# Kernel tuning notes

Measured on AMD Instinct MI355X. Metric: run time of the kernel, lower is better.

The kernel has to match this reference:

```python
import jax, jax.numpy as jnp
import numpy as np

B, N = 16, 2048
EMB_DIM = 512
K = 20          # neighbor_num
S = 1           # support_num

def _norm(x, axis):
    # F.normalize: x / max(||x||, 1e-12)
    return x / jnp.maximum(jnp.linalg.norm(x, axis=axis, keepdims=True), 1e-12)

def knn(verts, k):
    # verts: (b, v, 3); squared-distance knn excluding self
    inner = jnp.einsum('bvd,bwd->bvw', verts, verts)
    quad = jnp.sum(verts * verts, axis=2)
    dist = quad[:, :, None] - 2.0 * inner + quad[:, None, :]
    _, idx = jax.lax.top_k(-dist, k + 1)
    return idx[:, :, 1:]

def gather_nb(x, idx):
    # x: (b, v, c), idx: (b, v, n) -> (b, v, n, c)
    return jax.vmap(lambda t, i: t[i])(x, idx)

def dir_norm(verts, idx):
    d = gather_nb(verts, idx) - verts[:, :, None, :]
    return _norm(d, -1)

def conv_surface(idx, verts, directions, kernel_num):
    theta = jax.nn.relu(jnp.einsum('bvnd,dk->bvnk', dir_norm(verts, idx), _norm(directions, 0)))
    b, v, n, _ = theta.shape
    theta = theta.reshape(b, v, n, S, kernel_num)
    return jnp.sum(jnp.max(theta, axis=2), axis=2)  # (b, v, kernel_num)

def conv_layer(idx, verts, fm, w, bias, directions, out_ch):
    theta = jax.nn.relu(jnp.einsum('bvnd,dk->bvnk', dir_norm(verts, idx), _norm(directions, 0)))
    feat = fm @ w + bias                            # (b, v, (S+1)*out_ch)
    center = feat[:, :, :out_ch]
    support = gather_nb(feat[:, :, out_ch:], idx)   # (b, v, n, S*out_ch)
    b, v, n, _ = support.shape
    act = (theta * support).reshape(b, v, n, S, out_ch)
    return center + jnp.sum(jnp.max(act, axis=2), axis=2)

def pool_layer(verts, fm, key, pooling_rate=4, neighbor_num=4):
    b, v, _ = verts.shape
    idx = knn(verts, neighbor_num)
    pooled = jnp.max(gather_nb(fm, idx), axis=2)
    samp = jax.random.permutation(key, v)[: v // pooling_rate]
    return verts[:, samp, :], pooled[:, samp, :]

def _forward(xyz, w1, b1, w2, b2, w3, b3, w4, b4, fcw, fcb, dir0,
             wc1, bc1, dir1, wc2, bc2, dir2, wc3, bc3, dir3, wc4, bc4, dir4,
             clw1, clb1, bn_gamma, bn_beta, clw2, clb2):
    relu = jax.nn.relu
    # PointNet trunk (Conv1d with kernel 1 == per-point matmul)
    x = relu(jnp.einsum('oc,bcn->bon', w1, xyz) + b1[None, :, None])
    x = relu(jnp.einsum('oc,bcn->bon', w2, x) + b2[None, :, None])
    gf = jnp.max(x, axis=2, keepdims=True)
    x = jnp.concatenate([x, jnp.broadcast_to(gf, x.shape)], axis=1)
    x = relu(jnp.einsum('oc,bcn->bon', w3, x) + b3[None, :, None])
    x = relu(jnp.einsum('oc,bcn->bon', w4, x) + b4[None, :, None])
    x = jnp.max(x, axis=2)                          # (B, 1024)
    # GCN3D trunk
    verts = jnp.transpose(xyz, (0, 2, 1))           # (B, N, 3)
    idx = knn(verts, K)
    fm0 = relu(conv_surface(idx, verts, dir0, 32))
    fm1 = relu(conv_layer(idx, verts, fm0, wc1, bc1, dir1, 64))
    verts, fm1 = pool_layer(verts, fm1, jax.random.key(1))
    idx = knn(verts, K)
    fm2 = relu(conv_layer(idx, verts, fm1, wc2, bc2, dir2, 128))
    fm3 = relu(conv_layer(idx, verts, fm2, wc3, bc3, dir3, 256))
    verts, fm3 = pool_layer(verts, fm3, jax.random.key(2))
    idx = knn(verts, K)
    fm4 = conv_layer(idx, verts, fm3, wc4, bc4, dir4, 1024)
    fg = jnp.max(fm4, axis=1)                       # (B, 1024)
    fc_data = jnp.concatenate([x, fg], axis=1)      # (B, 2048)
    embedding = fc_data @ fcw.T + fcb
    # classifier, eval mode: Dropout -> identity; BN uses running mean 0 / var 1
    h = fc_data @ clw1.T + clb1
    h = relu(h / jnp.sqrt(1.0 + 1e-5) * bn_gamma + bn_beta)
    pred = h @ clw2.T + clb2
    return embedding, pred

def setup_inputs():
    key = jax.random.key(0)
    ks = jax.random.split(key, 32)
    rn = lambda k, shp: jax.random.normal(k, shp, dtype=jnp.float32) * 0.05
    return {
        'xyz': jax.random.normal(ks[0], (B, 3, N), dtype=jnp.float32),
        'w1': rn(ks[1], (64, 3)), 'b1': rn(ks[2], (64,)),
        'w2': rn(ks[3], (128, 64)), 'b2': rn(ks[4], (128,)),
        'w3': rn(ks[5], (256, 256)), 'b3': rn(ks[6], (256,)),
        'w4': rn(ks[7], (1024, 256)), 'b4': rn(ks[8], (1024,)),
        'fcw': rn(ks[9], (EMB_DIM, 2048)), 'fcb': rn(ks[10], (EMB_DIM,)),
        'dir0': rn(ks[11], (3, 32)),
        'wc1': rn(ks[12], (32, 128)), 'bc1': rn(ks[13], (128,)), 'dir1': rn(ks[14], (3, 64)),
        'wc2': rn(ks[15], (64, 256)), 'bc2': rn(ks[16], (256,)), 'dir2': rn(ks[17], (3, 128)),
        'wc3': rn(ks[18], (128, 512)), 'bc3': rn(ks[19], (512,)), 'dir3': rn(ks[20], (3, 256)),
        'wc4': rn(ks[21], (256, 2048)), 'bc4': rn(ks[22], (2048,)), 'dir4': rn(ks[23], (3, 1024)),
        'clw1': rn(ks[24], (512, 2048)), 'clb1': rn(ks[25], (512,)),
        'bn_gamma': jnp.ones((512,), dtype=jnp.float32),
        'bn_beta': jnp.zeros((512,), dtype=jnp.float32),
        'clw2': rn(ks[26], (6, 512)), 'clb2': rn(ks[27], (6,)),
    }

def reference(xyz, w1, b1, w2, b2, w3, b3, w4, b4, fcw, fcb, dir0, wc1, bc1, dir1, wc2, bc2, dir2, wc3, bc3, dir3, wc4, bc4, dir4, clw1, clb1, bn_gamma, bn_beta, clw2, clb2):
    return _forward(xyz, w1, b1, w2, b2, w3, b3, w4, b4, fcw, fcb, dir0, wc1, bc1, dir1, wc2, bc2, dir2, wc3, bc3, dir3, wc4, bc4, dir4, clw1, clb1, bn_gamma, bn_beta, clw2, clb2)
```

## Files before the change

### kernel.cpp

```cpp
#include <hip/hip_runtime.h>
#include <hip/hip_bf16.h>
#include <math.h>

#define BB 16
#define NN 2048

typedef __attribute__((ext_vector_type(8))) short s8v;
typedef __attribute__((ext_vector_type(4))) float f4v;

__global__ void k_sentinel(float* o, int n, float v){
  int i = blockIdx.x*256 + threadIdx.x;
  if (i < n) o[i] = v;
}

__device__ __forceinline__ ushort f2bf(float x){
  unsigned u = __float_as_uint(x);
  unsigned r = u + 0x7FFFu + ((u>>16)&1u);
  return (ushort)(r>>16);
}
__device__ __forceinline__ void splitbf(float v, ushort &h, ushort &l){
  h = f2bf(v);
  float hf = __uint_as_float((unsigned)h<<16);
  l = f2bf(v-hf);
}


__global__ void k_wsplit3(const float* __restrict__ s1, ushort* __restrict__ d1h, ushort* __restrict__ d1l, int n1,
                          const float* __restrict__ s2, ushort* __restrict__ d2h, ushort* __restrict__ d2l, int n2,
                          const float* __restrict__ s3, ushort* __restrict__ d3h, ushort* __restrict__ d3l, int n3){
  int id = blockIdx.x*256 + threadIdx.x;
  const float* s; ushort *dh, *dl; int i;
  if (id < n1){ s=s1; dh=d1h; dl=d1l; i=id; }
  else if (id < n1+n2){ s=s2; dh=d2h; dl=d2l; i=id-n1; }
  else if (id < n1+n2+n3){ s=s3; dh=d3h; dl=d3l; i=id-n1-n2; }
  else return;
  ushort h,l; splitbf(s[i], h, l);
  dh[i]=h; dl[i]=l;
}

__global__ void k_wstr4(const float* __restrict__ s1, ushort* __restrict__ d1h, ushort* __restrict__ d1l, int K1, int C1,
                        const float* __restrict__ s2, ushort* __restrict__ d2h, ushort* __restrict__ d2l, int K2, int C2,
                        const float* __restrict__ s3, ushort* __restrict__ d3h, ushort* __restrict__ d3l, int K3, int C3,
                        const float* __restrict__ s4, ushort* __restrict__ d4h, ushort* __restrict__ d4l, int K4, int C4){
  int id = blockIdx.x*256 + threadIdx.x;
  int n1=K1*C1, n2=K2*C2, n3=K3*C3, n4=K4*C4;
  const float* s; ushort *dh, *dl; int i, K, C;
  if (id < n1){ s=s1; dh=d1h; dl=d1l; i=id; K=K1; C=C1; }
  else if (id < n1+n2){ s=s2; dh=d2h; dl=d2l; i=id-n1; K=K2; C=C2; }
  else if (id < n1+n2+n3){ s=s3; dh=d3h; dl=d3l; i=id-n1-n2; K=K3; C=C3; }
  else if (id < n1+n2+n3+n4){ s=s4; dh=d4h; dl=d4l; i=id-n1-n2-n3; K=K4; C=C4; }
  else return;
  int c = i % C, k = i / C;
  ushort h,l; splitbf(s[i], h, l);
  dh[(size_t)c*K + k]=h; dl[(size_t)c*K + k]=l;
}


__global__ void k_mlp1s(const float* __restrict__ xyz, const float* __restrict__ w1,
                        const float* __restrict__ b1, ushort* __restrict__ xh,
                        ushort* __restrict__ xl){
  int id = blockIdx.x*256 + threadIdx.x;
  if (id >= BB*NN*64) return;
  int o = id & 63, n = (id>>6) & (NN-1), b = id>>17;
  float acc = b1[o];
  #pragma unroll
  for (int c=0;c<3;c++)
    acc += w1[o*3+c] * xyz[(size_t)(b*3+c)*NN + n];
  acc = fmaxf(acc, 0.f);
  ushort h,l; splitbf(acc, h, l);
  xh[id]=h; xl[id]=l;
}

__global__ void k_gmax(const float* __restrict__ pmax, ushort* __restrict__ gh,
                       ushort* __restrict__ gl, int parts, int total){
  int id = blockIdx.x*256 + threadIdx.x;
  if (id >= total) return;
  float m = pmax[(size_t)id*parts];
  for (int k=1;k<parts;k++) m = fmaxf(m, pmax[(size_t)id*parts+k]);
  ushort h,l; splitbf(m, h, l);
  gh[id]=h; gl[id]=l;
}

template<int EPI, int RELU, int BCOL>
__global__ __launch_bounds__(256) void k_bgemm(
    const ushort* __restrict__ Ahg, const ushort* __restrict__ Alg,
    const ushort* __restrict__ Bhg, const ushort* __restrict__ Blg,
    const ushort* __restrict__ gfh, const ushort* __restrict__ gfl,
    const float* __restrict__ bias,
    float* __restrict__ outp, float* __restrict__ pmaxp,
    ushort* __restrict__ oth, ushort* __restrict__ otl,
    int K, int ksplit, int Kb, int N, size_t sBT, size_t sOut, int M)
{
  __shared__ ushort Ah[128][40], Al[128][40];
  __shared__ ushort Bh[64][40],  Bl[64][40];
  __shared__ float red[2][128];
  int t = threadIdx.x, z = blockIdx.z;
  int o0 = blockIdx.y*128, n0 = blockIdx.x*64;
  int wid = t>>6, lane = t&63;
  int wm = wid>>1, wn = wid&1;
  int lr = lane&15, kg = lane>>4;

  f4v acc[4][2];
  #pragma unroll
  for (int i=0;i<4;i++)
    #pragma unroll
    for (int j=0;j<2;j++) acc[i][j] = (f4v){0.f,0.f,0.f,0.f};

  for (int k0=0; k0<K; k0+=32){
    __syncthreads();
    #pragma unroll
    for (int i=0;i<2;i++){
      int j = i*256+t, oo = j>>2, k8 = (j&3)*8;
      size_t sp = (size_t)(o0+oo)*K + k0 + k8;
      *(s8v*)&Ah[oo][k8] = *(const s8v*)(Ahg+sp);
      *(s8v*)&Al[oo][k8] = *(const s8v*)(Alg+sp);
    }
    {
      int nn = t>>2, k8 = (t&3)*8, gk = k0+k8;
      const ushort *sh, *sl;
      if (gk < ksplit){
        size_t sp = (size_t)z*sBT + (size_t)(n0+nn)*Kb + gk;
        sh = Bhg+sp; sl = Blg+sp;
      } else {
        size_t sp = (size_t)z*(K-ksplit) + (gk-ksplit);
        sh = gfh+sp; sl = gfl+sp;
      }
      *(s8v*)&Bh[nn][k8] = *(const s8v*)sh;
      *(s8v*)&Bl[nn][k8] = *(const s8v*)sl;
    }
    __syncthreads();

    s8v ah[4], al[4], bh[2], bl[2];
    #pragma unroll
    for (int mt=0;mt<4;mt++){
      int row = wm*64 + mt*16 + lr;
      ah[mt] = *(const s8v*)&Ah[row][kg*8];
      al[mt] = *(const s8v*)&Al[row][kg*8];
    }
    #pragma unroll
    for (int nt=0;nt<2;nt++){
      int col = wn*32 + nt*16 + lr;
      bh[nt] = *(const s8v*)&Bh[col][kg*8];
      bl[nt] = *(const s8v*)&Bl[col][kg*8];
    }
    #pragma unroll
    for (int mt=0;mt<4;mt++)
      #pragma unroll
      for (int nt=0;nt<2;nt++){
        acc[mt][nt] = __builtin_amdgcn_mfma_f32_16x16x32_bf16(ah[mt], bh[nt], acc[mt][nt], 0,0,0);
        acc[mt][nt] = __builtin_amdgcn_mfma_f32_16x16x32_bf16(ah[mt], bl[nt], acc[mt][nt], 0,0,0);
        acc[mt][nt] = __builtin_amdgcn_mfma_f32_16x16x32_bf16(al[mt], bh[nt], acc[mt][nt], 0,0,0);
      }
  }

  if (EPI == 1 || EPI == 4){
    #pragma unroll
    for (int mt=0;mt<4;mt++){
      #pragma unroll
      for (int e=0;e<4;e++){
        int row = o0 + wm*64 + mt*16 + kg*4 + e;
        float bv = bias[row];
        float v0 = fmaxf(acc[mt][0][e]+bv, 0.f);
        float v1 = fmaxf(acc[mt][1][e]+bv, 0.f);
        if (EPI == 4){
          int col0 = n0 + wn*32 + lr;
          ushort h,l;
          splitbf(v0, h, l);
          size_t p0 = ((size_t)z*N + col0)*(size_t)M + row;
          oth[p0]=h; otl[p0]=l;
          splitbf(v1, h, l);
          size_t p1 = ((size_t)z*N + col0+16)*(size_t)M + row;
          oth[p1]=h; otl[p1]=l;
        }
        float m = fmaxf(v0, v1);
        m = fmaxf(m, __shfl_xor(m, 1, 64));
        m = fmaxf(m, __shfl_xor(m, 2, 64));
        m = fmaxf(m, __shfl_xor(m, 4, 64));
        m = fmaxf(m, __shfl_xor(m, 8, 64));
        if (lr == 0) red[wn][wm*64 + mt*16 + kg*4 + e] = m;
      }
    }
    __syncthreads();
    if (t < 128){
      float m = fmaxf(red[0][t], red[1][t]);
      pmaxp[((size_t)z*M + o0 + t)*gridDim.x + blockIdx.x] = m;
    }
  } else {
    #pragma unroll
    for (int mt=0;mt<4;mt++){
      #pragma unroll
      for (int nt=0;nt<2;nt++){
        int col = n0 + wn*32 + nt*16 + lr;
        #pragma unroll
        for (int e=0;e<4;e++){
          int row = o0 + wm*64 + mt*16 + kg*4 + e;
          float bv = BCOL ? bias[col] : bias[row];
          float v = acc[mt][nt][e] + bv;
          if (RELU) v = fmaxf(v, 0.f);
          if (EPI == 0)
            outp[(size_t)z*sOut + (size_t)row*N + col] = v;
          if (EPI == 3){
            ushort h,l; splitbf(v, h, l);
            size_t p = ((size_t)z*N + col)*(size_t)M + row;
            oth[p]=h; otl[p]=l;
          }
        }
      }
    }
  }
}

__global__ void k_xmax(const float* __restrict__ pmax, float* __restrict__ xmax){
  int id = blockIdx.x*256 + threadIdx.x;
  if (id >= BB*1024) return;
  float m = pmax[(size_t)id*32];
  for (int k=1;k<32;k++) m = fmaxf(m, pmax[(size_t)id*32+k]);
  xmax[id] = m;
}


#define TF2BODY \
  unsigned ks2 = 0x1BD11BDAu ^ k0 ^ k1; \
  unsigned a = x0 + k0, b = x1 + k1; \
  { \
  a += b; b = (b<<13)|(b>>19); b ^= a; \
  a += b; b = (b<<15)|(b>>17); b ^= a; \
  a += b; b = (b<<26)|(b>>6);  b ^= a; \
  a += b; b = (b<<6) |(b>>26); b ^= a;  a += k1;  b += ks2 + 1u; \
  a += b; b = (b<<17)|(b>>15); b ^= a; \
  a += b; b = (b<<29)|(b>>3);  b ^= a; \
  a += b; b = (b<<16)|(b>>16); b ^= a; \
  a += b; b = (b<<24)|(b>>8);  b ^= a;  a += ks2; b += k0  + 2u; \
  a += b; b = (b<<13)|(b>>19); b ^= a; \
  a += b; b = (b<<15)|(b>>17); b ^= a; \
  a += b; b = (b<<26)|(b>>6);  b ^= a; \
  a += b; b = (b<<6) |(b>>26); b ^= a;  a += k0;  b += k1  + 3u; \
  a += b; b = (b<<17)|(b>>15); b ^= a; \
  a += b; b = (b<<29)|(b>>3);  b ^= a; \
  a += b; b = (b<<16)|(b>>16); b ^= a; \
  a += b; b = (b<<24)|(b>>8);  b ^= a;  a += k1;  b += ks2 + 4u; \
  a += b; b = (b<<13)|(b>>19); b ^= a; \
  a += b; b = (b<<15)|(b>>17); b ^= a; \
  a += b; b = (b<<26)|(b>>6);  b ^= a; \
  a += b; b = (b<<6) |(b>>26); b ^= a;  a += ks2; b += k0  + 5u; \
  } \
  o0 = a; o1 = b;

__device__ __forceinline__ void tf2(unsigned k0, unsigned k1, unsigned x0, unsigned x1,
                                    unsigned &o0, unsigned &o1){ TF2BODY }
static void tf2h(unsigned k0, unsigned k1, unsigned x0, unsigned x1,
                 unsigned &o0, unsigned &o1){ TF2BODY }

__global__ void k_permkeys3(unsigned a0, unsigned a1, unsigned* __restrict__ ka,
                            unsigned b0, unsigned b1, unsigned* __restrict__ kb,
                            unsigned c0, unsigned c1, unsigned* __restrict__ kc){
  int id = blockIdx.x*256 + threadIdx.x;
  if (id < 2048){ unsigned x,y; tf2(a0,a1, 0u,(unsigned)id, x,y); ka[id] = x^y; }
  if (id < 2048){ unsigned x,y; tf2(b0,b1, 0u,(unsigned)id, x,y); kb[id] = x^y; }
  if (id < 512){ unsigned x,y; tf2(c0,c1, 0u,(unsigned)id, x,y); kc[id] = x^y; }
}

__global__ void k_permrank(int n, const unsigned* __restrict__ keys,
                           const int* __restrict__ vin, int* __restrict__ vout){
  int i = blockIdx.x*256 + threadIdx.x;
  if (i >= n) return;
  unsigned ki = keys[i];
  int rank = 0;
  for (int j=0;j<n;j++){
    unsigned kj = keys[j];
    rank += (kj < ki) || (kj == ki && j < i);
  }
  vout[rank] = vin ? vin[i] : i;
}


__global__ void k_transpose(const float* __restrict__ xyz, float* __restrict__ verts){
  int id = blockIdx.x*256 + threadIdx.x;
  if (id >= BB*NN*3) return;
  int c = id % 3, v = (id/3) % NN, b = id/(3*NN);
  verts[id] = xyz[(size_t)(b*3+c)*NN + v];
}

template<int CPL, int KSEL>
__global__ __launch_bounds__(256,4) void k_knn_s(const float* __restrict__ vbcs,
                                                 int numQ, int* __restrict__ out){
  constexpr int V = CPL*64;
  constexpr int GS = (CPL < 8) ? CPL : 8;
  constexpr int NG = CPL/GS;
  int t = threadIdx.x, wid = t>>6, lane = t&63;
  int b = blockIdx.y;
  int q = blockIdx.x*4 + wid;
  if (q >= numQ) return;
  const float* vx = vbcs + (size_t)b*3*V;
  const float* vy = vx + V;
  const float* vz = vy + V;
  float qx = vx[q], qy = vy[q], qz = vz[q];
  float qq = qx*qx + qy*qy + qz*qz;
  unsigned d[CPL];
  #pragma unroll
  for (int i=0;i<CPL;i++){
    int c = lane + i*64;
    float wx=vx[c], wy=vy[c], wz=vz[c];
    float inner = qx*wx + qy*wy + qz*wz;
    float ww = wx*wx + wy*wy + wz*wz;
    float dd = qq - 2.f*inner + ww;
    unsigned db = __float_as_uint(dd);
    d[i] = (db & 0x80000000u) ? ~db : (db | 0x80000000u);
  }
  unsigned long long g[NG];
  #pragma unroll
  for (int gg=0; gg<NG; gg++){
    unsigned long long m = ~0ull;
    #pragma unroll
    for (int j=0;j<GS;j++){
      int p = gg*GS+j;
      unsigned long long kk = ((unsigned long long)d[p]<<32) | (unsigned)p;
      m = (kk<m)?kk:m;
    }
    g[gg] = m;
  }
  unsigned lmin = (unsigned)(g[0]>>32);
  #pragma unroll
  for (int gg=1;gg<NG;gg++){ unsigned x = (unsigned)(g[gg]>>32); lmin = (x<lmin)?x:lmin; }

  int* orow = out + ((size_t)b*numQ + q)*KSEL;
  for (int r=0; r<=KSEL; r++){
    unsigned bd = lmin;
    #pragma unroll
    for (int off=32; off>0; off>>=1){
      unsigned o = __shfl_xor(bd, off, 64);
      bd = (o < bd) ? o : bd;
    }
    unsigned long long bal = __ballot(lmin == bd);
    int winner = __ffsll(bal) - 1;
    if (lane == winner){
      unsigned long long mbest = g[0];
      #pragma unroll
      for (int gg=1;gg<NG;gg++) mbest = (g[gg]<mbest)?g[gg]:mbest;
      int pos = (int)(mbest & 0xffffffffull);
      if (r>0) orow[r-1] = lane + pos*64;
      int gi = pos / GS;
      #pragma unroll
      for (int gg=0; gg<NG; gg++){
        if (gg == gi){
          unsigned long long m = ~0ull;
          #pragma unroll
          for (int j=0;j<GS;j++){
            int p = gg*GS+j;
            unsigned long long kk = ((unsigned long long)d[p]<<32) | (unsigned)p;
            if (kk <= mbest) kk = ~0ull;
            m = (kk<m)?kk:m;
          }
          g[gg] = m;
        }
      }
      unsigned nl = (unsigned)(g[0]>>32);
      #pragma unroll
      for (int gg=1;gg<NG;gg++){ unsigned x = (unsigned)(g[gg]>>32); nl = (x<nl)?x:nl; }
      lmin = nl;
    }
  }
}

__global__ void k_poolidx(const int* __restrict__ idxsrc, const int* __restrict__ perm,
                          int* __restrict__ outp, int Vsrc, int numS, int total){
  int id = blockIdx.x*256 + threadIdx.x;
  if (id >= total) return;
  int j = id & 3, s = (id>>2) % numS, b = id/(numS*4);
  outp[id] = idxsrc[((size_t)b*Vsrc + perm[s])*20 + j];
}

__global__ void k_dirs(const float* __restrict__ verts, int V, const int* __restrict__ idx,
                       float* __restrict__ dirs, int total){
  int id = blockIdx.x*256 + threadIdx.x;
  if (id >= total) return;
  int v = (id/20) % V, b = id/(20*V);
  const float* vb = verts + (size_t)b*V*3;
  int nb = idx[id];
  float dx = vb[nb*3+0]-vb[v*3+0];
  float dy = vb[nb*3+1]-vb[v*3+1];
  float dz = vb[nb*3+2]-vb[v*3+2];
  float s = 1.f / fmaxf(sqrtf(dx*dx+dy*dy+dz*dz), 1e-12f);
  dirs[(size_t)id*3+0]=dx*s; dirs[(size_t)id*3+1]=dy*s; dirs[(size_t)id*3+2]=dz*s;
}

__global__ void k_surf(const float* __restrict__ dirs, const float* __restrict__ dir0,
                       ushort* __restrict__ fh, ushort* __restrict__ fl, int V){
  int id = blockIdx.x*256 + threadIdx.x;
  if (id >= BB*V*32) return;
  int k = id & 31; int vv = (id>>5) % V; int b = id/(32*V);
  float nx=dir0[k], ny=dir0[32+k], nz=dir0[64+k];
  float s = 1.f/fmaxf(sqrtf(nx*nx+ny*ny+nz*nz), 1e-12f);
  nx*=s; ny*=s; nz*=s;
  const float* dd = dirs + (size_t)(b*V+vv)*60;
  float m = 0.f;
  for (int n=0;n<20;n++){
    float th = dd[n*3]*nx + dd[n*3+1]*ny + dd[n*3+2]*nz;
    m = fmaxf(m, fmaxf(th, 0.f));
  }
  ushort h,l; splitbf(m, h, l);
  size_t p = (size_t)(b*V+vv)*32 + k;
  fh[p]=h; fl[p]=l;
}

template<int OUT>
__global__ void k_comb(const float* __restrict__ feat, const int* __restrict__ idx,
                       const float* __restrict__ dirs, const float* __restrict__ dw,
                       float* __restrict__ outp, ushort* __restrict__ oh, ushort* __restrict__ ol,
                       int V, int OC, int relu_flag){
  int id = blockIdx.x*256 + threadIdx.x;
  if (id >= BB*V*OC) return;
  int oc = id % OC, v = (id/OC) % V, b = id/(OC*V);
  float wx=dw[oc], wy=dw[OC+oc], wz=dw[2*OC+oc];
  float s = 1.f/fmaxf(sqrtf(wx*wx+wy*wy+wz*wz), 1e-12f);
  wx*=s; wy*=s; wz*=s;
  size_t row = (size_t)b*V + v;
  const int* ir = idx + row*20;
  const float* dd = dirs + row*60;
  float center = feat[row*2*OC + oc];
  float m = -INFINITY;
  for (int n=0;n<20;n++){
    int nb = ir[n];
    float th = dd[n*3]*wx + dd[n*3+1]*wy + dd[n*3+2]*wz;
    th = fmaxf(th, 0.f);
    float sup = feat[((size_t)b*V + nb)*2*OC + OC + oc];
    m = fmaxf(m, th*sup);
  }
  float rv = center + m;
  if (OUT == 0){
    outp[row*OC + oc] = relu_flag ? fmaxf(rv, 0.f) : rv;
  } else {
    rv = fmaxf(rv, 0.f);
    ushort h,l; splitbf(rv, h, l);
    oh[row*OC + oc]=h; ol[row*OC + oc]=l;
  }
}

template<int OUT>
__global__ void k_pool(const float* __restrict__ fm, const int* __restrict__ idx4,
                       float* __restrict__ outp, ushort* __restrict__ oh, ushort* __restrict__ ol,
                       int V, int C, int numS){
  int id = blockIdx.x*256 + threadIdx.x;
  if (id >= BB*numS*C) return;
  int c = id % C, sI = (id/C) % numS, b = id/(C*numS);
  const int* ir = idx4 + ((size_t)b*numS + sI)*4;
  float m = -INFINITY;
  for (int n=0;n<4;n++) m = fmaxf(m, fm[((size_t)b*V + ir[n])*C + c]);
  size_t p = ((size_t)b*numS + sI)*C + c;
  if (OUT == 0) outp[p] = m;
  else { ushort h,l; splitbf(m, h, l); oh[p]=h; ol[p]=l; }
}

__global__ void k_vgather(const float* __restrict__ vin, const int* __restrict__ perm,
                          float* __restrict__ vout, float* __restrict__ vbcs,
                          int V, int numS){
  int id = blockIdx.x*256 + threadIdx.x;
  if (id >= BB*numS*3) return;
  int c = id % 3, sI = (id/3) % numS, b = id/(3*numS);
  float val = vin[((size_t)b*V + perm[sI])*3 + c];
  vout[id] = val;
  vbcs[((size_t)b*3 + c)*numS + sI] = val;
}

__global__ void k_colmax(const float* __restrict__ x, float* __restrict__ o, int Vr, int C){
  int id = blockIdx.x*256 + threadIdx.x;
  if (id >= BB*C) return;
  int c = id % C, b = id / C;
  float m = -INFINITY;
  for (int v=0; v<Vr; v++) m = fmaxf(m, x[(size_t)(b*Vr+v)*C + c]);
  o[id] = m;
}


__global__ __launch_bounds__(256) void k_emb2(const float* __restrict__ xmax, const float* __restrict__ fg,
                                              const float* __restrict__ fcw, const float* __restrict__ fcb,
                                              float* __restrict__ outp){
  int gid = blockIdx.x*4 + (threadIdx.x>>6);
  int lane = threadIdx.x & 63;
  if (gid >= BB*512) return;
  int e = gid & 511, b = gid >> 9;
  const float* wr = fcw + (size_t)e*2048;
  const float* xb = xmax + b*1024;
  const float* gb = fg + b*1024;
  float acc = 0.f;
  for (int k=lane; k<1024; k+=64)
    acc += xb[k]*wr[k] + gb[k]*wr[1024+k];
  #pragma unroll
  for (int off=32; off>0; off>>=1) acc += __shfl_xor(acc, off, 64);
  if (lane==0) outp[gid] = acc + fcb[e];
}

__global__ __launch_bounds__(256) void k_h2(const float* __restrict__ xmax, const float* __restrict__ fg,
                                            const float* __restrict__ clw1, const float* __restrict__ clb1,
                                            const float* __restrict__ gamma, const float* __restrict__ beta,
                                            float* __restrict__ h){
  int gid = blockIdx.x*4 + (threadIdx.x>>6);
  int lane = threadIdx.x & 63;
  if (gid >= BB*512) return;
  int j = gid & 511, b = gid >> 9;
  const float* wr = clw1 + (size_t)j*2048;
  const float* xb = xmax + b*1024;
  const float* gb = fg + b*1024;
  float acc = 0.f;
  for (int k=lane; k<1024; k+=64)
    acc += xb[k]*wr[k] + gb[k]*wr[1024+k];
  #pragma unroll
  for (int off=32; off>0; off>>=1) acc += __shfl_xor(acc, off, 64);
  if (lane==0){
    const float inv_s = 1.0f / sqrtf(1.0f + 1e-5f);
    float v = (acc + clb1[j]) * inv_s * gamma[j] + beta[j];
    h[gid] = fmaxf(v, 0.f);
  }
}

__global__ __launch_bounds__(256) void k_pred2(const float* __restrict__ h, const float* __restrict__ clw2,
                                               const float* __restrict__ clb2, float* __restrict__ outp){
  int gid = blockIdx.x*4 + (threadIdx.x>>6);
  int lane = threadIdx.x & 63;
  if (gid >= BB*6) return;
  int o = gid % 6, b = gid / 6;
  const float* hb = h + b*512;
  const float* wr = clw2 + o*512;
  float acc = 0.f;
  for (int k=lane; k<512; k+=64) acc += hb[k]*wr[k];
  #pragma unroll
  for (int off=32; off>0; off>>=1) acc += __shfl_xor(acc, off, 64);
  if (lane==0) outp[BB*512 + gid] = acc + clb2[o];
}


static inline int cdiv(long long a, int b){ return (int)((a + b - 1)/b); }

extern "C" void kernel_launch(void* const* d_in, const int* in_sizes, int n_in,
                              void* d_out, int out_size, void* d_ws, size_t ws_size,
                              hipStream_t stream){
  float* out = (float*)d_out;
  if (n_in != 30 || in_sizes[0] != BB*3*NN || out_size != BB*512 + BB*6){
    k_sentinel<<<cdiv(out_size,256),256,0,stream>>>(out, out_size, 2000.0f);
    return;
  }
  const float* xyz  = (const float*)d_in[0];
  const float* w1   = (const float*)d_in[1];
  const float* b1   = (const float*)d_in[2];
  const float* w2   = (const float*)d_in[3];
  const float* b2   = (const float*)d_in[4];
  const float* w3   = (const float*)d_in[5];
  const float* b3   = (const float*)d_in[6];
  const float* w4   = (const float*)d_in[7];
  const float* b4   = (const float*)d_in[8];
  const float* fcw  = (const float*)d_in[9];
  const float* fcb  = (const float*)d_in[10];
  const float* dir0 = (const float*)d_in[11];
  const float* wc1  = (const float*)d_in[12];
  const float* bc1  = (const float*)d_in[13];
  const float* dir1 = (const float*)d_in[14];
  const float* wc2  = (const float*)d_in[15];
  const float* bc2  = (const float*)d_in[16];
  const float* dir2 = (const float*)d_in[17];
  const float* wc3  = (const float*)d_in[18];
  const float* bc3  = (const float*)d_in[19];
  const float* dir3 = (const float*)d_in[20];
  const float* wc4  = (const float*)d_in[21];
  const float* bc4  = (const float*)d_in[22];
  const float* dir4 = (const float*)d_in[23];
  const float* clw1 = (const float*)d_in[24];
  const float* clb1 = (const float*)d_in[25];
  const float* gma  = (const float*)d_in[26];
  const float* bta  = (const float*)d_in[27];
  const float* clw2 = (const float*)d_in[28];
  const float* clb2 = (const float*)d_in[29];

  char* w = (char*)d_ws;
  size_t off = 0;
  auto A = [&](size_t bytes){ size_t r = off; off += (bytes + 255) & ~(size_t)255; return r; };
  const size_t oXMAX = A((size_t)BB*1024*4);
  const size_t oFG   = A((size_t)BB*1024*4);
  const size_t oGFP  = A((size_t)BB*128*2*2);
  const size_t oH    = A((size_t)BB*512*4);
  const size_t oP2048= A(2048*4);
  const size_t oP512 = A(512*4);
  const size_t oPK1  = A(2048*4);
  const size_t oPK2  = A(2048*4);
  const size_t oPK3  = A(512*4);
  const size_t oPA   = A(2048*4);
  const size_t oPMAX = A((size_t)BB*1024*32*4);
  const size_t oV0   = A((size_t)BB*2048*3*4);
  const size_t oV1   = A((size_t)BB*512*3*4);
  const size_t oV2   = A((size_t)BB*128*3*4);
  const size_t oV1S  = A((size_t)BB*3*512*4);
  const size_t oV2S  = A((size_t)BB*3*128*4);
  const size_t oIDX0 = A((size_t)BB*2048*20*4);
  const size_t oDIR0 = A((size_t)BB*2048*20*3*4);
  const size_t oFM0  = A((size_t)BB*2048*32*2*2);
  const size_t oFM1  = A((size_t)BB*2048*64*4);
  const size_t oI40  = A((size_t)BB*512*4*4);
  const size_t oFM1P = A((size_t)BB*512*64*2*2);
  const size_t oIDX1 = A((size_t)BB*512*20*4);
  const size_t oDIR1 = A((size_t)BB*512*20*3*4);
  const size_t oFM2  = A((size_t)BB*512*128*2*2);
  const size_t oFM3  = A((size_t)BB*512*256*4);
  const size_t oI41  = A((size_t)BB*128*4*4);
  const size_t oFM3P = A((size_t)BB*128*256*2*2);
  const size_t oIDX2 = A((size_t)BB*128*20*4);
  const size_t oDIR2 = A((size_t)BB*128*20*3*4);
  const size_t oFM4  = A((size_t)BB*128*1024*4);
  const size_t oBIGA = A((size_t)BB*256*NN*4);
  const size_t oBIGB = A((size_t)BB*128*NN*4);
  const size_t oW2P  = A((size_t)128*64*2*2);
  const size_t oW3P  = A((size_t)256*256*2*2);
  const size_t oW4P  = A((size_t)1024*256*2*2);
  const size_t oWC1T = A((size_t)32*128*2*2);
  const size_t oWC2T = A((size_t)64*256*2*2);
  const size_t oWC3T = A((size_t)128*512*2*2);
  const size_t oWC4T = A((size_t)256*2048*2*2);
  if (off > ws_size){
    k_sentinel<<<cdiv(out_size,256),256,0,stream>>>(out, out_size, 1000.0f);
    return;
  }
  float* xmax = (float*)(w+oXMAX); float* fg = (float*)(w+oFG);
  float* hbuf = (float*)(w+oH);
  ushort* gfh = (ushort*)(w+oGFP); ushort* gfl = gfh + BB*128;
  int* p2048 = (int*)(w+oP2048);   int* p512 = (int*)(w+oP512);
  unsigned* pk1 = (unsigned*)(w+oPK1); unsigned* pk2 = (unsigned*)(w+oPK2);
  unsigned* pk3 = (unsigned*)(w+oPK3); int* pa = (int*)(w+oPA);
  float* pmax = (float*)(w+oPMAX);
  float* v0 = (float*)(w+oV0); float* v1 = (float*)(w+oV1); float* v2 = (float*)(w+oV2);
  float* v1s = (float*)(w+oV1S); float* v2s = (float*)(w+oV2S);
  int* idx0 = (int*)(w+oIDX0); int* idx1 = (int*)(w+oIDX1); int* idx2 = (int*)(w+oIDX2);
  int* i40 = (int*)(w+oI40);   int* i41 = (int*)(w+oI41);
  float* d0 = (float*)(w+oDIR0); float* d1 = (float*)(w+oDIR1); float* d2 = (float*)(w+oDIR2);
  ushort* fm0h = (ushort*)(w+oFM0); ushort* fm0l = fm0h + (size_t)BB*2048*32;
  float* fm1 = (float*)(w+oFM1);
  ushort* fm1ph = (ushort*)(w+oFM1P); ushort* fm1pl = fm1ph + (size_t)BB*512*64;
  ushort* fm2h = (ushort*)(w+oFM2); ushort* fm2l = fm2h + (size_t)BB*512*128;
  float* fm3 = (float*)(w+oFM3);
  ushort* fm3ph = (ushort*)(w+oFM3P); ushort* fm3pl = fm3ph + (size_t)BB*128*256;
  float* fm4 = (float*)(w+oFM4);
  ushort* x1h = (ushort*)(w+oBIGA); ushort* x1l = x1h + (size_t)BB*2048*64;
  ushort* x3h = (ushort*)(w+oBIGA); ushort* x3l = x3h + (size_t)BB*2048*256;
  ushort* x2h = (ushort*)(w+oIDX0); ushort* x2l = x2h + (size_t)BB*2048*128;
  float* feat = (float*)(w+oBIGB);
  ushort* w2ph = (ushort*)(w+oW2P); ushort* w2pl = w2ph + 128*64;
  ushort* w3ph = (ushort*)(w+oW3P); ushort* w3pl = w3ph + 256*256;
  ushort* w4ph = (ushort*)(w+oW4P); ushort* w4pl = w4ph + 1024*256;
  ushort* wc1h = (ushort*)(w+oWC1T); ushort* wc1l = wc1h + 32*128;
  ushort* wc2h = (ushort*)(w+oWC2T); ushort* wc2l = wc2h + 64*256;
  ushort* wc3h = (ushort*)(w+oWC3T); ushort* wc3l = wc3h + 128*512;
  ushort* wc4h = (ushort*)(w+oWC4T); ushort* wc4l = wc4h + 256*2048;

  k_wsplit3<<<cdiv(128*64+256*256+1024*256,256),256,0,stream>>>(
      w2, w2ph, w2pl, 128*64,  w3, w3ph, w3pl, 256*256,  w4, w4ph, w4pl, 1024*256);
  k_wstr4<<<cdiv(32*128+64*256+128*512+256*2048,256),256,0,stream>>>(
      wc1, wc1h, wc1l, 32, 128,  wc2, wc2h, wc2l, 64, 256,
      wc3, wc3h, wc3l, 128, 512, wc4, wc4h, wc4l, 256, 2048);

  k_mlp1s<<<cdiv((long long)BB*NN*64,256),256,0,stream>>>(xyz, w1, b1, x1h, x1l);
  k_bgemm<4,1,0><<<dim3(32,1,BB),256,0,stream>>>(w2ph, w2pl, x1h, x1l, nullptr, nullptr,
      b2, nullptr, pmax, x2h, x2l, 64, 64, 64, 2048, (size_t)2048*64, 0, 128);
  k_gmax<<<cdiv(BB*128,256),256,0,stream>>>(pmax, gfh, gfl, 32, BB*128);
  k_bgemm<3,1,0><<<dim3(32,2,BB),256,0,stream>>>(w3ph, w3pl, x2h, x2l, gfh, gfl,
      b3, nullptr, nullptr, x3h, x3l, 256, 128, 128, 2048, (size_t)2048*128, 0, 256);
  k_bgemm<1,1,0><<<dim3(32,8,BB),256,0,stream>>>(w4ph, w4pl, x3h, x3l, nullptr, nullptr,
      b4, nullptr, pmax, nullptr, nullptr, 256, 256, 256, 2048, (size_t)2048*256, 0, 1024);
  k_xmax<<<cdiv(BB*1024,256),256,0,stream>>>(pmax, xmax);

  {
    unsigned ck0=0u, ck1=1u, nk0,nk1, s00,s01, s10,s11, sc0,sc1;
    tf2h(ck0,ck1, 0u,0u, nk0,nk1);
    tf2h(ck0,ck1, 0u,1u, s00,s01);
    tf2h(nk0,nk1, 0u,1u, s10,s11);
    tf2h(0u,2u,  0u,1u, sc0,sc1);
    k_permkeys3<<<8,256,0,stream>>>(s00,s01,pk1, s10,s11,pk2, sc0,sc1,pk3);
    k_permrank<<<8,256,0,stream>>>(2048, pk1, nullptr, pa);
    k_permrank<<<8,256,0,stream>>>(2048, pk2, pa, p2048);
    k_permrank<<<2,256,0,stream>>>(512, pk3, nullptr, p512);
  }

  k_transpose<<<cdiv((long long)BB*NN*3,256),256,0,stream>>>(xyz, v0);
  k_knn_s<32,20><<<dim3(512,BB),256,0,stream>>>(xyz, 2048, idx0);
  k_dirs<<<cdiv((long long)BB*2048*20,256),256,0,stream>>>(v0, 2048, idx0, d0, BB*2048*20);
  k_surf<<<cdiv((long long)BB*2048*32,256),256,0,stream>>>(d0, dir0, fm0h, fm0l, 2048);
  k_bgemm<0,0,1><<<dim3(2,256,1),256,0,stream>>>(fm0h, fm0l, wc1h, wc1l, nullptr, nullptr,
      bc1, feat, nullptr, nullptr, nullptr, 32, 32, 32, 128, 0, 0, BB*2048);
  k_comb<0><<<cdiv((long long)BB*2048*64,256),256,0,stream>>>(feat, idx0, d0, dir1, fm1, nullptr, nullptr, 2048, 64, 1);
  k_poolidx<<<cdiv(BB*512*4,256),256,0,stream>>>(idx0, p2048, i40, 2048, 512, BB*512*4);
  k_pool<1><<<cdiv((long long)BB*512*64,256),256,0,stream>>>(fm1, i40, nullptr, fm1ph, fm1pl, 2048, 64, 512);
  k_vgather<<<cdiv((long long)BB*512*3,256),256,0,stream>>>(v0, p2048, v1, v1s, 2048, 512);
  k_knn_s<8,20><<<dim3(128,BB),256,0,stream>>>(v1s, 512, idx1);
  k_dirs<<<cdiv((long long)BB*512*20,256),256,0,stream>>>(v1, 512, idx1, d1, BB*512*20);
  k_bgemm<0,0,1><<<dim3(4,64,1),256,0,stream>>>(fm1ph, fm1pl, wc2h, wc2l, nullptr, nullptr,
      bc2, feat, nullptr, nullptr, nullptr, 64, 64, 64, 256, 0, 0, BB*512);
  k_comb<1><<<cdiv((long long)BB*512*128,256),256,0,stream>>>(feat, idx1, d1, dir2, nullptr, fm2h, fm2l, 512, 128, 1);
  k_bgemm<0,0,1><<<dim3(8,64,1),256,0,stream>>>(fm2h, fm2l, wc3h, wc3l, nullptr, nullptr,
      bc3, feat, nullptr, nullptr, nullptr, 128, 128, 128, 512, 0, 0, BB*512);
  k_comb<0><<<cdiv((long long)BB*512*256,256),256,0,stream>>>(feat, idx1, d1, dir3, fm3, nullptr, nullptr, 512, 256, 1);
  k_poolidx<<<cdiv(BB*128*4,256),256,0,stream>>>(idx1, p512, i41, 512, 128, BB*128*4);
  k_pool<1><<<cdiv((long long)BB*128*256,256),256,0,stream>>>(fm3, i41, nullptr, fm3ph, fm3pl, 512, 256, 128);
  k_vgather<<<cdiv((long long)BB*128*3,256),256,0,stream>>>(v1, p512, v2, v2s, 512, 128);
  k_knn_s<2,20><<<dim3(32,BB),256,0,stream>>>(v2s, 128, idx2);
  k_dirs<<<cdiv((long long)BB*128*20,256),256,0,stream>>>(v2, 128, idx2, d2, BB*128*20);
  k_bgemm<0,0,1><<<dim3(32,16,1),256,0,stream>>>(fm3ph, fm3pl, wc4h, wc4l, nullptr, nullptr,
      bc4, feat, nullptr, nullptr, nullptr, 256, 256, 256, 2048, 0, 0, BB*128);
  k_comb<0><<<cdiv((long long)BB*128*1024,256),256,0,stream>>>(feat, idx2, d2, dir4, fm4, nullptr, nullptr, 128, 1024, 0);
  k_colmax<<<cdiv(BB*1024,256),256,0,stream>>>(fm4, fg, 128, 1024);

  k_emb2<<<cdiv(BB*512,4),256,0,stream>>>(xmax, fg, fcw, fcb, out);
  k_h2<<<cdiv(BB*512,4),256,0,stream>>>(xmax, fg, clw1, clb1, gma, bta, hbuf);
  k_pred2<<<cdiv(BB*6,4),256,0,stream>>>(hbuf, clw2, clb2, out);
}
```

Baseline: 718.1 us.

## Fuse direction computation into kNN and vectorize surface/combine kernels by four

The kNN kernel now writes the normalized neighbor directions as it selects each neighbor. This removes the separate k_dirs and k_transpose kernels and the vertex-major copies. Vertex gathers now emit only the channel-major layout. k_surf and k_comb become 4-wide variants in which each thread handles four output channels with float4 loads, so direction and index reads are shared across the four channels. The cost is a few extra scalar loads and stores per winner lane inside the kNN selection loop, and more registers per thread in the combine kernel.

Measured after the change: 739.0 us. 1.03x slower.

```diff
diff --git a/kernel.cpp b/kernel.cpp
--- a/kernel.cpp
+++ b/kernel.cpp
@@ -274,16 +274,10 @@
 }
 
 
-__global__ void k_transpose(const float* __restrict__ xyz, float* __restrict__ verts){
-  int id = blockIdx.x*256 + threadIdx.x;
-  if (id >= BB*NN*3) return;
-  int c = id % 3, v = (id/3) % NN, b = id/(3*NN);
-  verts[id] = xyz[(size_t)(b*3+c)*NN + v];
-}
-
 template<int CPL, int KSEL>
 __global__ __launch_bounds__(256,4) void k_knn_s(const float* __restrict__ vbcs,
-                                                 int numQ, int* __restrict__ out){
+                                                 int numQ, int* __restrict__ out,
+                                                 float* __restrict__ dirs){
   constexpr int V = CPL*64;
   constexpr int GS = (CPL < 8) ? CPL : 8;
   constexpr int NG = CPL/GS;
@@ -324,6 +318,7 @@
   for (int gg=1;gg<NG;gg++){ unsigned x = (unsigned)(g[gg]>>32); lmin = (x<lmin)?x:lmin; }
 
   int* orow = out + ((size_t)b*numQ + q)*KSEL;
+  float* drow = dirs + ((size_t)b*numQ + q)*(KSEL*3);
   for (int r=0; r<=KSEL; r++){
     unsigned bd = lmin;
     #pragma unroll
@@ -338,7 +333,15 @@
       #pragma unroll
       for (int gg=1;gg<NG;gg++) mbest = (g[gg]<mbest)?g[gg]:mbest;
       int pos = (int)(mbest & 0xffffffffull);
-      if (r>0) orow[r-1] = lane + pos*64;
+      if (r>0){
+        int c = lane + pos*64;
+        orow[r-1] = c;
+        float dx = vx[c]-qx, dy = vy[c]-qy, dz = vz[c]-qz;
+        float s = 1.f / fmaxf(sqrtf(dx*dx+dy*dy+dz*dz), 1e-12f);
+        drow[(r-1)*3+0] = dx*s;
+        drow[(r-1)*3+1] = dy*s;
+        drow[(r-1)*3+2] = dz*s;
+      }
       int gi = pos / GS;
       #pragma unroll
       for (int gg=0; gg<NG; gg++){
@@ -370,69 +373,84 @@
   outp[id] = idxsrc[((size_t)b*Vsrc + perm[s])*20 + j];
 }
 
-__global__ void k_dirs(const float* __restrict__ verts, int V, const int* __restrict__ idx,
-                       float* __restrict__ dirs, int total){
-  int id = blockIdx.x*256 + threadIdx.x;
-  if (id >= total) return;
-  int v = (id/20) % V, b = id/(20*V);
-  const float* vb = verts + (size_t)b*V*3;
-  int nb = idx[id];
-  float dx = vb[nb*3+0]-vb[v*3+0];
-  float dy = vb[nb*3+1]-vb[v*3+1];
-  float dz = vb[nb*3+2]-vb[v*3+2];
-  float s = 1.f / fmaxf(sqrtf(dx*dx+dy*dy+dz*dz), 1e-12f);
-  dirs[(size_t)id*3+0]=dx*s; dirs[(size_t)id*3+1]=dy*s; dirs[(size_t)id*3+2]=dz*s;
-}
-
-__global__ void k_surf(const float* __restrict__ dirs, const float* __restrict__ dir0,
-                       ushort* __restrict__ fh, ushort* __restrict__ fl, int V){
-  int id = blockIdx.x*256 + threadIdx.x;
-  if (id >= BB*V*32) return;
-  int k = id & 31; int vv = (id>>5) % V; int b = id/(32*V);
-  float nx=dir0[k], ny=dir0[32+k], nz=dir0[64+k];
-  float s = 1.f/fmaxf(sqrtf(nx*nx+ny*ny+nz*nz), 1e-12f);
-  nx*=s; ny*=s; nz*=s;
+__global__ void k_surf4(const float* __restrict__ dirs, const float* __restrict__ dir0,
+                        ushort* __restrict__ fh, ushort* __restrict__ fl, int V){
+  int id = blockIdx.x*256 + threadIdx.x;
+  if (id >= BB*V*8) return;
+  int k4 = (id & 7)*4; int vv = (id>>3) % V; int b = id/(8*V);
+  f4v nx = *(const f4v*)&dir0[k4];
+  f4v ny = *(const f4v*)&dir0[32+k4];
+  f4v nz = *(const f4v*)&dir0[64+k4];
+  #pragma unroll
+  for (int j=0;j<4;j++){
+    float s = 1.f/fmaxf(sqrtf(nx[j]*nx[j]+ny[j]*ny[j]+nz[j]*nz[j]), 1e-12f);
+    nx[j]*=s; ny[j]*=s; nz[j]*=s;
+  }
   const float* dd = dirs + (size_t)(b*V+vv)*60;
-  float m = 0.f;
+  f4v m = (f4v){0.f,0.f,0.f,0.f};
   for (int n=0;n<20;n++){
-    float th = dd[n*3]*nx + dd[n*3+1]*ny + dd[n*3+2]*nz;
-    m = fmaxf(m, fmaxf(th, 0.f));
-  }
-  ushort h,l; splitbf(m, h, l);
-  size_t p = (size_t)(b*V+vv)*32 + k;
-  fh[p]=h; fl[p]=l;
+    float d0=dd[n*3], d1=dd[n*3+1], d2=dd[n*3+2];
+    #pragma unroll
+    for (int j=0;j<4;j++){
+      float th = d0*nx[j] + d1*ny[j] + d2*nz[j];
+      m[j] = fmaxf(m[j], fmaxf(th, 0.f));
+    }
+  }
+  size_t p = (size_t)(b*V+vv)*32 + k4;
+  #pragma unroll
+  for (int j=0;j<4;j++){
+    ushort h,l; splitbf(m[j], h, l);
+    fh[p+j]=h; fl[p+j]=l;
+  }
 }
 
 template<int OUT>
-__global__ void k_comb(const float* __restrict__ feat, const int* __restrict__ idx,
-                       const float* __restrict__ dirs, const float* __restrict__ dw,
-                       float* __restrict__ outp, ushort* __restrict__ oh, ushort* __restrict__ ol,
-                       int V, int OC, int relu_flag){
-  int id = blockIdx.x*256 + threadIdx.x;
-  if (id >= BB*V*OC) return;
-  int oc = id % OC, v = (id/OC) % V, b = id/(OC*V);
-  float wx=dw[oc], wy=dw[OC+oc], wz=dw[2*OC+oc];
-  float s = 1.f/fmaxf(sqrtf(wx*wx+wy*wy+wz*wz), 1e-12f);
-  wx*=s; wy*=s; wz*=s;
+__global__ void k_comb4(const float* __restrict__ feat, const int* __restrict__ idx,
+                        const float* __restrict__ dirs, const float* __restrict__ dw,
+                        float* __restrict__ outp, ushort* __restrict__ oh, ushort* __restrict__ ol,
+                        int V, int OC, int relu_flag){
+  int id = blockIdx.x*256 + threadIdx.x;
+  int OC4 = OC>>2;
+  if (id >= BB*V*OC4) return;
+  int o4 = (id % OC4)*4, v = (id/OC4) % V, b = id/(OC4*V);
+  f4v wx = *(const f4v*)&dw[o4];
+  f4v wy = *(const f4v*)&dw[OC+o4];
+  f4v wz = *(const f4v*)&dw[2*OC+o4];
+  #pragma unroll
+  for (int j=0;j<4;j++){
+    float s = 1.f/fmaxf(sqrtf(wx[j]*wx[j]+wy[j]*wy[j]+wz[j]*wz[j]), 1e-12f);
+    wx[j]*=s; wy[j]*=s; wz[j]*=s;
+  }
   size_t row = (size_t)b*V + v;
   const int* ir = idx + row*20;
   const float* dd = dirs + row*60;
-  float center = feat[row*2*OC + oc];
-  float m = -INFINITY;
+  f4v center = *(const f4v*)&feat[row*2*OC + o4];
+  f4v m = (f4v){-INFINITY,-INFINITY,-INFINITY,-INFINITY};
   for (int n=0;n<20;n++){
     int nb = ir[n];
-    float th = dd[n*3]*wx + dd[n*3+1]*wy + dd[n*3+2]*wz;
-    th = fmaxf(th, 0.f);
-    float sup = feat[((size_t)b*V + nb)*2*OC + OC + oc];
-    m = fmaxf(m, th*sup);
-  }
-  float rv = center + m;
+    float d0=dd[n*3], d1=dd[n*3+1], d2=dd[n*3+2];
+    f4v sup = *(const f4v*)&feat[((size_t)b*V + nb)*2*OC + OC + o4];
+    #pragma unroll
+    for (int j=0;j<4;j++){
+      float th = fmaxf(d0*wx[j] + d1*wy[j] + d2*wz[j], 0.f);
+      m[j] = fmaxf(m[j], th*sup[j]);
+    }
+  }
   if (OUT == 0){
-    outp[row*OC + oc] = relu_flag ? fmaxf(rv, 0.f) : rv;
+    f4v rv;
+    #pragma unroll
+    for (int j=0;j<4;j++){
+      float x = center[j] + m[j];
+      rv[j] = relu_flag ? fmaxf(x, 0.f) : x;
+    }
+    *(f4v*)&outp[row*OC + o4] = rv;
   } else {
-    rv = fmaxf(rv, 0.f);
-    ushort h,l; splitbf(rv, h, l);
-    oh[row*OC + oc]=h; ol[row*OC + oc]=l;
+    #pragma unroll
+    for (int j=0;j<4;j++){
+      float x = fmaxf(center[j] + m[j], 0.f);
+      ushort h,l; splitbf(x, h, l);
+      oh[row*OC + o4 + j]=h; ol[row*OC + o4 + j]=l;
+    }
   }
 }
 
@@ -451,15 +469,12 @@
   else { ushort h,l; splitbf(m, h, l); oh[p]=h; ol[p]=l; }
 }
 
-__global__ void k_vgather(const float* __restrict__ vin, const int* __restrict__ perm,
-                          float* __restrict__ vout, float* __restrict__ vbcs,
-                          int V, int numS){
-  int id = blockIdx.x*256 + threadIdx.x;
-  if (id >= BB*numS*3) return;
-  int c = id % 3, sI = (id/3) % numS, b = id/(3*numS);
-  float val = vin[((size_t)b*V + perm[sI])*3 + c];
-  vout[id] = val;
-  vbcs[((size_t)b*3 + c)*numS + sI] = val;
+__global__ void k_vgather(const float* __restrict__ vsrc, const int* __restrict__ perm,
+                          float* __restrict__ vbcs, int V, int numS){
+  int id = blockIdx.x*256 + threadIdx.x;
+  if (id >= BB*3*numS) return;
+  int s = id % numS, c = (id/numS) % 3, b = id/(3*numS);
+  vbcs[id] = vsrc[((size_t)b*3 + c)*V + perm[s]];
 }
 
 __global__ void k_colmax(const float* __restrict__ x, float* __restrict__ o, int Vr, int C){
@@ -584,9 +599,6 @@
   const size_t oPK3  = A(512*4);
   const size_t oPA   = A(2048*4);
   const size_t oPMAX = A((size_t)BB*1024*32*4);
-  const size_t oV0   = A((size_t)BB*2048*3*4);
-  const size_t oV1   = A((size_t)BB*512*3*4);
-  const size_t oV2   = A((size_t)BB*128*3*4);
   const size_t oV1S  = A((size_t)BB*3*512*4);
   const size_t oV2S  = A((size_t)BB*3*128*4);
   const size_t oIDX0 = A((size_t)BB*2048*20*4);
@@ -624,7 +636,6 @@
   unsigned* pk1 = (unsigned*)(w+oPK1); unsigned* pk2 = (unsigned*)(w+oPK2);
   unsigned* pk3 = (unsigned*)(w+oPK3); int* pa = (int*)(w+oPA);
   float* pmax = (float*)(w+oPMAX);
-  float* v0 = (float*)(w+oV0); float* v1 = (float*)(w+oV1); float* v2 = (float*)(w+oV2);
   float* v1s = (float*)(w+oV1S); float* v2s = (float*)(w+oV2S);
   int* idx0 = (int*)(w+oIDX0); int* idx1 = (int*)(w+oIDX1); int* idx2 = (int*)(w+oIDX2);
   int* i40 = (int*)(w+oI40);   int* i41 = (int*)(w+oI41);
@@ -676,32 +687,28 @@
     k_permrank<<<2,256,0,stream>>>(512, pk3, nullptr, p512);
   }
 
-  k_transpose<<<cdiv((long long)BB*NN*3,256),256,0,stream>>>(xyz, v0);
-  k_knn_s<32,20><<<dim3(512,BB),256,0,stream>>>(xyz, 2048, idx0);
-  k_dirs<<<cdiv((long long)BB*2048*20,256),256,0,stream>>>(v0, 2048, idx0, d0, BB*2048*20);
-  k_surf<<<cdiv((long long)BB*2048*32,256),256,0,stream>>>(d0, dir0, fm0h, fm0l, 2048);
+  k_knn_s<32,20><<<dim3(512,BB),256,0,stream>>>(xyz, 2048, idx0, d0);
+  k_surf4<<<cdiv((long long)BB*2048*8,256),256,0,stream>>>(d0, dir0, fm0h, fm0l, 2048);
   k_bgemm<0,0,1><<<dim3(2,256,1),256,0,stream>>>(fm0h, fm0l, wc1h, wc1l, nullptr, nullptr,
       bc1, feat, nullptr, nullptr, nullptr, 32, 32, 32, 128, 0, 0, BB*2048);
-  k_comb<0><<<cdiv((long long)BB*2048*64,256),256,0,stream>>>(feat, idx0, d0, dir1, fm1, nullptr, nullptr, 2048, 64, 1);
+  k_comb4<0><<<cdiv((long long)BB*2048*16,256),256,0,stream>>>(feat, idx0, d0, dir1, fm1, nullptr, nullptr, 2048, 64, 1);
   k_poolidx<<<cdiv(BB*512*4,256),256,0,stream>>>(idx0, p2048, i40, 2048, 512, BB*512*4);
   k_pool<1><<<cdiv((long long)BB*512*64,256),256,0,stream>>>(fm1, i40, nullptr, fm1ph, fm1pl, 2048, 64, 512);
-  k_vgather<<<cdiv((long long)BB*512*3,256),256,0,stream>>>(v0, p2048, v1, v1s, 2048, 512);
-  k_knn_s<8,20><<<dim3(128,BB),256,0,stream>>>(v1s, 512, idx1);
-  k_dirs<<<cdiv((long long)BB*512*20,256),256,0,stream>>>(v1, 512, idx1, d1, BB*512*20);
+  k_vgather<<<cdiv((long long)BB*3*512,256),256,0,stream>>>(xyz, p2048, v1s, 2048, 512);
+  k_knn_s<8,20><<<dim3(128,BB),256,0,stream>>>(v1s, 512, idx1, d1);
   k_bgemm<0,0,1><<<dim3(4,64,1),256,0,stream>>>(fm1ph, fm1pl, wc2h, wc2l, nullptr, nullptr,
       bc2, feat, nullptr, nullptr, nullptr, 64, 64, 64, 256, 0, 0, BB*512);
-  k_comb<1><<<cdiv((long long)BB*512*128,256),256,0,stream>>>(feat, idx1, d1, dir2, nullptr, fm2h, fm2l, 512, 128, 1);
+  k_comb4<1><<<cdiv((long long)BB*512*32,256),256,0,stream>>>(feat, idx1, d1, dir2, nullptr, fm2h, fm2l, 512, 128, 1);
   k_bgemm<0,0,1><<<dim3(8,64,1),256,0,stream>>>(fm2h, fm2l, wc3h, wc3l, nullptr, nullptr,
       bc3, feat, nullptr, nullptr, nullptr, 128, 128, 128, 512, 0, 0, BB*512);
-  k_comb<0><<<cdiv((long long)BB*512*256,256),256,0,stream>>>(feat, idx1, d1, dir3, fm3, nullptr, nullptr, 512, 256, 1);
+  k_comb4<0><<<cdiv((long long)BB*512*64,256),256,0,stream>>>(feat, idx1, d1, dir3, fm3, nullptr, nullptr, 512, 256, 1);
   k_poolidx<<<cdiv(BB*128*4,256),256,0,stream>>>(idx1, p512, i41, 512, 128, BB*128*4);
   k_pool<1><<<cdiv((long long)BB*128*256,256),256,0,stream>>>(fm3, i41, nullptr, fm3ph, fm3pl, 512, 256, 128);
-  k_vgather<<<cdiv((long long)BB*128*3,256),256,0,stream>>>(v1, p512, v2, v2s, 512, 128);
-  k_knn_s<2,20><<<dim3(32,BB),256,0,stream>>>(v2s, 128, idx2);
-  k_dirs<<<cdiv((long long)BB*128*20,256),256,0,stream>>>(v2, 128, idx2, d2, BB*128*20);
+  k_vgather<<<cdiv((long long)BB*3*128,256),256,0,stream>>>(v1s, p512, v2s, 512, 128);
+  k_knn_s<2,20><<<dim3(32,BB),256,0,stream>>>(v2s, 128, idx2, d2);
   k_bgemm<0,0,1><<<dim3(32,16,1),256,0,stream>>>(fm3ph, fm3pl, wc4h, wc4l, nullptr, nullptr,
       bc4, feat, nullptr, nullptr, nullptr, 256, 256, 256, 2048, 0, 0, BB*128);
-  k_comb<0><<<cdiv((long long)BB*128*1024,256),256,0,stream>>>(feat, idx2, d2, dir4, fm4, nullptr, nullptr, 128, 1024, 0);
+  k_comb4<0><<<cdiv((long long)BB*128*256,256),256,0,stream>>>(feat, idx2, d2, dir4, fm4, nullptr, nullptr, 128, 1024, 0);
   k_colmax<<<cdiv(BB*1024,256),256,0,stream>>>(fm4, fg, 128, 1024);
 
   k_emb2<<<cdiv(BB*512,4),256,0,stream>>>(xmax, fg, fcw, fcb, out);
```
